# Kernel tuning notes

Measured on AMD Instinct MI355X. Metric: run time of the kernel, lower is better.

## Reference

```python
import jax, jax.numpy as jnp
import numpy as np

N_NODES = 100000
N_EDGES = 1600000
D_FEAT = 64
NUM_LAYERS = 4  # -> num_gcn_layers = 3


def spmm(edge_row, edge_col, edge_vals, x, n_nodes):
    # out[r] = sum_{e: row[e]==r} vals[e] * x[col[e]]
    gathered = edge_vals[:, None] * x[edge_col]  # [E, d]
    return jax.ops.segment_sum(gathered, edge_row, num_segments=n_nodes)


def setup_inputs() -> dict:
    key = jax.random.key(0)
    k1, k2, k3, k4 = jax.random.split(key, 4)
    x = jax.random.normal(k1, (N_NODES, D_FEAT), dtype=jnp.float32)
    edge_row = jax.random.randint(k2, (N_EDGES,), 0, N_NODES, dtype=jnp.int32)
    edge_col = jax.random.randint(k3, (N_EDGES,), 0, N_NODES, dtype=jnp.int32)
    edge_vals = jax.random.uniform(k4, (N_EDGES,), dtype=jnp.float32)
    return {"x": x, "edge_row": edge_row, "edge_col": edge_col, "edge_vals": edge_vals}


def reference(x, edge_row, edge_col, edge_vals):
    # resSumGCN: h_{i+1} = A h_i ; return sum_{i=1..L} h_i
    num_gcn_layers = NUM_LAYERS - 1
    h = x
    acc = jnp.zeros_like(x)
    for _ in range(num_gcn_layers):  # small fixed layer count
        h = spmm(edge_row, edge_col, edge_vals, h, N_NODES)
        acc = acc + h
    return acc
```

## Files before the change

kernel.cpp:

```cpp
#include <hip/hip_runtime.h>

#define N_NODES 100000
#define N_EDGES 1600000
#define D_FEAT  64

#define RSHIFT 8
#define RPB    256
#define NBK    ((N_NODES + RPB - 1) / RPB)
#define CAP    5120
#define EPB    4096
#define KBLK   ((N_EDGES + EPB - 1) / EPB)
#define OROW   (NBK + 1)
#define CVB    ((N_NODES * D_FEAT / 4 + 1023) / 1024)

typedef float f32x2 __attribute__((ext_vector_type(2)));

__device__ __forceinline__ unsigned short f2bf(float f) {
  union { float f; unsigned int i; } v; v.f = f;
  unsigned int b = v.i;
  return (unsigned short)((b + 0x7FFFu + ((b >> 16) & 1u)) >> 16);
}
__device__ __forceinline__ float ulo(int u) { return __int_as_float(u << 16); }
__device__ __forceinline__ float uhi(int u) { return __int_as_float(u & 0xFFFF0000); }
__device__ __forceinline__ f32x2 upk(int u) {
  f32x2 r; r.x = ulo(u); r.y = uhi(u); return r;
}
__device__ __forceinline__ int pk(float a, float b) {
  return (int)f2bf(a) | ((int)f2bf(b) << 16);
}

__global__ __launch_bounds__(1024) void convert_bin(
    const float4* __restrict__ xin, ushort4* __restrict__ xout,
    const int* __restrict__ erow, const int* __restrict__ ecol,
    const float* __restrict__ evals, int2* __restrict__ tmp,
    int* __restrict__ offs) {
  __shared__ int hist[NBK];
  __shared__ int sc[NBK];
  int t = threadIdx.x;
  int k = blockIdx.x;
  if (k >= KBLK) {
    int i = (k - KBLK) * 1024 + t;
    if (i < N_NODES * D_FEAT / 4) {
      float4 v = xin[i];
      ushort4 o;
      o.x = f2bf(v.x); o.y = f2bf(v.y); o.z = f2bf(v.z); o.w = f2bf(v.w);
      xout[i] = o;
    }
    return;
  }
  if (t < NBK) hist[t] = 0;
  __syncthreads();
  int base = k * EPB;
  int nk = N_EDGES - base; if (nk > EPB) nk = EPB;
  int key[4], vb[4], rk[4], bk[4];
#pragma unroll
  for (int j = 0; j < 4; ++j) {
    int li = j * 1024 + t;
    bk[j] = -1;
    if (li < nk) {
      int e = base + li;
      int r = erow[e];
      key[j] = ((r & (RPB - 1)) << 17) | ecol[e];
      vb[j]  = __float_as_int(evals[e]);
      bk[j]  = r >> RSHIFT;
      rk[j]  = atomicAdd(&hist[bk[j]], 1);
    }
  }
  __syncthreads();
  if (t < NBK) sc[t] = hist[t];
  __syncthreads();
  for (int off = 1; off < NBK; off <<= 1) {
    int u = (t >= off && t < NBK) ? sc[t - off] : 0;
    __syncthreads();
    if (t < NBK) sc[t] += u;
    __syncthreads();
  }
  if (t < NBK) {
    int ex = sc[t] - hist[t];
    sc[t] = ex;
    offs[k * OROW + t] = ex;
  }
  if (t == 0) offs[k * OROW + NBK] = nk;
  __syncthreads();
#pragma unroll
  for (int j = 0; j < 4; ++j) {
    if (bk[j] >= 0) {
      int pos = sc[bk[j]] + rk[j];
      tmp[k * EPB + pos] = make_int2(key[j], vb[j]);
    }
  }
}

__global__ __launch_bounds__(256) void build_csr(
    const int2* __restrict__ tmp, const int* __restrict__ offs,
    int2* __restrict__ edges, int* __restrict__ row_beg,
    int* __restrict__ row_end) {
  __shared__ int hist[RPB];
  __shared__ int cur[RPB];
  int b = blockIdx.x;
  int t = threadIdx.x;
  int oct = t >> 3;
  int ol  = t & 7;
  hist[t] = 0;
  __syncthreads();
  for (int k = oct; k < KBLK; k += 32) {
    int o0 = offs[k * OROW + b];
    int o1 = offs[k * OROW + b + 1];
    const int2* seg = tmp + k * EPB;
    for (int i = o0 + ol; i < o1; i += 8)
      atomicAdd(&hist[seg[i].x >> 17], 1);
  }
  __syncthreads();
  int v  = hist[t];
  int v2 = (v + 1) & ~1;
  cur[t] = v2;
  __syncthreads();
  for (int off = 1; off < 256; off <<= 1) {
    int u = (t >= off) ? cur[t - off] : 0;
    __syncthreads();
    cur[t] += u;
    __syncthreads();
  }
  int excl2 = cur[t] - v2;
  int base = b * CAP;
  int gr = b * RPB + t;
  if (gr < N_NODES) {
    row_beg[gr] = base + excl2;
    row_end[gr] = base + excl2 + v;
  }
  if (v & 1) edges[base + excl2 + v] = make_int2(0, 0);
  __syncthreads();
  cur[t] = excl2;
  __syncthreads();
  for (int k = oct; k < KBLK; k += 32) {
    int o0 = offs[k * OROW + b];
    int o1 = offs[k * OROW + b + 1];
    const int2* seg = tmp + k * EPB;
    for (int i = o0 + ol; i < o1; i += 8) {
      int2 ed = seg[i];
      int pos = atomicAdd(&cur[ed.x >> 17], 1);
      edges[base + pos] = make_int2(ed.x & 0x1FFFF, ed.y);
    }
  }
}

__global__ __launch_bounds__(256) void spmm_oct(
    const int* __restrict__ row_beg, const int* __restrict__ row_end,
    const int2* __restrict__ edges, const int4* __restrict__ xq,
    int4* __restrict__ h_q, float4* __restrict__ out,
    const int4* __restrict__ add1, const int4* __restrict__ add2,
    int final_mode) {
  int t = threadIdx.x;
  int lane = t & 63;
  int oct = lane >> 3;
  int ol  = lane & 7;
  int row = blockIdx.x * 32 + (t >> 6) * 8 + oct;
  int e0 = row_beg[row];
  int e1 = row_end[row];
  const int4* ep = (const int4*)edges + (e0 >> 1);
  int npair = (e1 - e0 + 1) >> 1;
  f32x2 c0 = {0.f, 0.f}, c1 = {0.f, 0.f}, c2 = {0.f, 0.f}, c3 = {0.f, 0.f};

#define PAIR(m) { \
    int4 g0 = xq[(size_t)(m).x * 8 + ol]; \
    int4 g1 = xq[(size_t)(m).z * 8 + ol]; \
    float v0 = __int_as_float((m).y), v1 = __int_as_float((m).w); \
    f32x2 vv0 = {v0, v0}, vv1 = {v1, v1}; \
    c0 += vv0 * upk(g0.x) + vv1 * upk(g1.x); \
    c1 += vv0 * upk(g0.y) + vv1 * upk(g1.y); \
    c2 += vv0 * upk(g0.z) + vv1 * upk(g1.z); \
    c3 += vv0 * upk(g0.w) + vv1 * upk(g1.w); \
  }

  int p = 0;
  for (; p + 2 <= npair; p += 2) {
    int4 m0 = ep[p];
    int4 m1 = ep[p + 1];
    PAIR(m0);
    PAIR(m1);
  }
  if (p < npair) {
    int4 m0 = ep[p];
    PAIR(m0);
  }
#undef PAIR

  size_t oi = (size_t)row * 8 + ol;
  if (final_mode) {
    int4 r1 = add1[oi];
    int4 r2 = add2[oi];
    float4 lo, hi;
    lo.x = c0.x + ulo(r1.x) + ulo(r2.x);
    lo.y = c0.y + uhi(r1.x) + uhi(r2.x);
    lo.z = c1.x + ulo(r1.y) + ulo(r2.y);
    lo.w = c1.y + uhi(r1.y) + uhi(r2.y);
    hi.x = c2.x + ulo(r1.z) + ulo(r2.z);
    hi.y = c2.y + uhi(r1.z) + uhi(r2.z);
    hi.z = c3.x + ulo(r1.w) + ulo(r2.w);
    hi.w = c3.y + uhi(r1.w) + uhi(r2.w);
    out[(size_t)row * 16 + ol * 2]     = lo;
    out[(size_t)row * 16 + ol * 2 + 1] = hi;
  } else {
    int4 pq;
    pq.x = pk(c0.x, c0.y);
    pq.y = pk(c1.x, c1.y);
    pq.z = pk(c2.x, c2.y);
    pq.w = pk(c3.x, c3.y);
    h_q[oi] = pq;
  }
}

extern "C" void kernel_launch(void* const* d_in, const int* in_sizes, int n_in,
                              void* d_out, int out_size, void* d_ws, size_t ws_size,
                              hipStream_t stream) {
  const float* x     = (const float*)d_in[0];
  const int*   erow  = (const int*)d_in[1];
  const int*   ecol  = (const int*)d_in[2];
  const float* evals = (const float*)d_in[3];
  float* out = (float*)d_out;

  const size_t hb_bytes   = (size_t)N_NODES * D_FEAT * 2;
  const size_t ecap_bytes = (size_t)NBK * CAP * sizeof(int2);
  char* ws = (char*)d_ws;
  int4*    xbf  = (int4*)   (ws);
  int4*    bufA = (int4*)   (ws + hb_bytes);
  int2*    tmp  = (int2*)   (ws + hb_bytes);
  int4*    bufB = (int4*)   (ws + 2 * hb_bytes);
  int*     offs = (int*)    (ws + 2 * hb_bytes);
  int2* edges   = (int2*)(ws + 3 * hb_bytes);
  int* row_beg  = (int*) (ws + 3 * hb_bytes + ecap_bytes);
  int* row_end  = (int*) (ws + 3 * hb_bytes + ecap_bytes + 400000);

  const int sblocks = N_NODES / 32;

  convert_bin<<<KBLK + CVB, 1024, 0, stream>>>(
      (const float4*)x, (ushort4*)xbf, erow, ecol, evals, tmp, offs);
  build_csr<<<NBK, 256, 0, stream>>>(tmp, offs, edges, row_beg, row_end);

  spmm_oct<<<sblocks, 256, 0, stream>>>(row_beg, row_end, edges, xbf,
                                        bufA, nullptr, nullptr, nullptr, 0);
  spmm_oct<<<sblocks, 256, 0, stream>>>(row_beg, row_end, edges, bufA,
                                        bufB, nullptr, nullptr, nullptr, 0);
  spmm_oct<<<sblocks, 256, 0, stream>>>(row_beg, row_end, edges, bufB,
                                        nullptr, (float4*)out, bufA, bufB, 1);
}
```

Before: 226.1 us.

## Count per-row degrees with global atomics during binning and halve bucket size

Per-row edge counts are now accumulated with global atomics in convert_bin, into a counter array zeroed by a new memset. This lets build_csr drop its first full pass over the binned edges, which only built a shared-memory histogram. Buckets shrink from 256 to 128 rows, with a smaller per-bucket capacity, which doubles the number of build_csr blocks. The cost is 1.6M scattered global atomics plus an extra memset, and bucket overflow becomes more likely if a bucket's degrees are skewed.

After: 273.6 us. 1.21x slower.

```diff
diff --git a/kernel.cpp b/kernel.cpp
--- a/kernel.cpp
+++ b/kernel.cpp
@@ -4,10 +4,10 @@
 #define N_EDGES 1600000
 #define D_FEAT  64
 
-#define RSHIFT 8
-#define RPB    256
+#define RSHIFT 7
+#define RPB    128
 #define NBK    ((N_NODES + RPB - 1) / RPB)
-#define CAP    5120
+#define CAP    2816
 #define EPB    4096
 #define KBLK   ((N_EDGES + EPB - 1) / EPB)
 #define OROW   (NBK + 1)
@@ -33,7 +33,7 @@
     const float4* __restrict__ xin, ushort4* __restrict__ xout,
     const int* __restrict__ erow, const int* __restrict__ ecol,
     const float* __restrict__ evals, int2* __restrict__ tmp,
-    int* __restrict__ offs) {
+    int* __restrict__ offs, int* __restrict__ gcnt) {
   __shared__ int hist[NBK];
   __shared__ int sc[NBK];
   int t = threadIdx.x;
@@ -64,6 +64,7 @@
       vb[j]  = __float_as_int(evals[e]);
       bk[j]  = r >> RSHIFT;
       rk[j]  = atomicAdd(&hist[bk[j]], 1);
+      atomicAdd(&gcnt[r], 1);
     }
   }
   __syncthreads();
@@ -93,45 +94,40 @@
 
 __global__ __launch_bounds__(256) void build_csr(
     const int2* __restrict__ tmp, const int* __restrict__ offs,
-    int2* __restrict__ edges, int* __restrict__ row_beg,
-    int* __restrict__ row_end) {
-  __shared__ int hist[RPB];
+    const int* __restrict__ gcnt, int2* __restrict__ edges,
+    int* __restrict__ row_beg, int* __restrict__ row_end) {
   __shared__ int cur[RPB];
+  __shared__ int sc[RPB];
   int b = blockIdx.x;
   int t = threadIdx.x;
+  int v = 0, v2 = 0;
+  if (t < RPB) {
+    int g = b * RPB + t;
+    v = (g < N_NODES) ? gcnt[g] : 0;
+    v2 = (v + 1) & ~1;
+    sc[t] = v2;
+  }
+  __syncthreads();
+  for (int off = 1; off < RPB; off <<= 1) {
+    int u = (t >= off && t < RPB) ? sc[t - off] : 0;
+    __syncthreads();
+    if (t < RPB) sc[t] += u;
+    __syncthreads();
+  }
+  if (t < RPB) {
+    int excl2 = sc[t] - v2;
+    cur[t] = excl2;
+    int g = b * RPB + t;
+    int base = b * CAP;
+    if (g < N_NODES) {
+      row_beg[g] = base + excl2;
+      row_end[g] = base + excl2 + v;
+    }
+    if (v & 1) edges[base + excl2 + v] = make_int2(0, 0);
+  }
+  __syncthreads();
   int oct = t >> 3;
   int ol  = t & 7;
-  hist[t] = 0;
-  __syncthreads();
-  for (int k = oct; k < KBLK; k += 32) {
-    int o0 = offs[k * OROW + b];
-    int o1 = offs[k * OROW + b + 1];
-    const int2* seg = tmp + k * EPB;
-    for (int i = o0 + ol; i < o1; i += 8)
-      atomicAdd(&hist[seg[i].x >> 17], 1);
-  }
-  __syncthreads();
-  int v  = hist[t];
-  int v2 = (v + 1) & ~1;
-  cur[t] = v2;
-  __syncthreads();
-  for (int off = 1; off < 256; off <<= 1) {
-    int u = (t >= off) ? cur[t - off] : 0;
-    __syncthreads();
-    cur[t] += u;
-    __syncthreads();
-  }
-  int excl2 = cur[t] - v2;
-  int base = b * CAP;
-  int gr = b * RPB + t;
-  if (gr < N_NODES) {
-    row_beg[gr] = base + excl2;
-    row_end[gr] = base + excl2 + v;
-  }
-  if (v & 1) edges[base + excl2 + v] = make_int2(0, 0);
-  __syncthreads();
-  cur[t] = excl2;
-  __syncthreads();
   for (int k = oct; k < KBLK; k += 32) {
     int o0 = offs[k * OROW + b];
     int o1 = offs[k * OROW + b + 1];
@@ -139,7 +135,7 @@
     for (int i = o0 + ol; i < o1; i += 8) {
       int2 ed = seg[i];
       int pos = atomicAdd(&cur[ed.x >> 17], 1);
-      edges[base + pos] = make_int2(ed.x & 0x1FFFF, ed.y);
+      edges[b * CAP + pos] = make_int2(ed.x & 0x1FFFF, ed.y);
     }
   }
 }
@@ -222,20 +218,22 @@
   const size_t hb_bytes   = (size_t)N_NODES * D_FEAT * 2;
   const size_t ecap_bytes = (size_t)NBK * CAP * sizeof(int2);
   char* ws = (char*)d_ws;
-  int4*    xbf  = (int4*)   (ws);
-  int4*    bufA = (int4*)   (ws + hb_bytes);
-  int2*    tmp  = (int2*)   (ws + hb_bytes);
-  int4*    bufB = (int4*)   (ws + 2 * hb_bytes);
-  int*     offs = (int*)    (ws + 2 * hb_bytes);
-  int2* edges   = (int2*)(ws + 3 * hb_bytes);
-  int* row_beg  = (int*) (ws + 3 * hb_bytes + ecap_bytes);
-  int* row_end  = (int*) (ws + 3 * hb_bytes + ecap_bytes + 400000);
+  int4* xbf   = (int4*)(ws);
+  int4* bufA  = (int4*)(ws + hb_bytes);
+  int2* tmp   = (int2*)(ws + hb_bytes);
+  int4* bufB  = (int4*)(ws + 2 * hb_bytes);
+  int*  offs  = (int*) (ws + 2 * hb_bytes);
+  int2* edges = (int2*)(ws + 3 * hb_bytes);
+  int*  row_beg = (int*)(ws + 3 * hb_bytes + ecap_bytes);
+  int*  row_end = (int*)(ws + 3 * hb_bytes + ecap_bytes + 400000);
+  int*  gcnt    = (int*)(ws + 3 * hb_bytes + ecap_bytes + 800000);
 
   const int sblocks = N_NODES / 32;
 
+  hipMemsetAsync(gcnt, 0, (size_t)N_NODES * sizeof(int), stream);
   convert_bin<<<KBLK + CVB, 1024, 0, stream>>>(
-      (const float4*)x, (ushort4*)xbf, erow, ecol, evals, tmp, offs);
-  build_csr<<<NBK, 256, 0, stream>>>(tmp, offs, edges, row_beg, row_end);
+      (const float4*)x, (ushort4*)xbf, erow, ecol, evals, tmp, offs, gcnt);
+  build_csr<<<NBK, 256, 0, stream>>>(tmp, offs, gcnt, edges, row_beg, row_end);
 
   spmm_oct<<<sblocks, 256, 0, stream>>>(row_beg, row_end, edges, xbf,
                                         bufA, nullptr, nullptr, nullptr, 0);
```
